# Kernel tuning notes

Measured on AMD Instinct MI355X. Metric: run time of the kernel, lower is better.

## Reference

```python
import jax, jax.numpy as jnp
import numpy as np

N_HEADS = 16
D_MODEL = 1024
D_K = D_MODEL // N_HEADS


def setup_inputs() -> dict:
    key = jax.random.key(0)
    ks = jax.random.split(key, 7)
    B, S = 2, 2048
    init = 0.02
    return {
        "query": jax.random.normal(ks[0], (B, S, D_MODEL), dtype=jnp.float32),
        "key": jax.random.normal(ks[1], (B, S, D_MODEL), dtype=jnp.float32),
        "value": jax.random.normal(ks[2], (B, S, D_MODEL), dtype=jnp.float32),
        "W_q": jax.random.normal(ks[3], (D_MODEL, D_MODEL), dtype=jnp.float32) * init,
        "W_k": jax.random.normal(ks[4], (D_MODEL, D_MODEL), dtype=jnp.float32) * init,
        "W_v": jax.random.normal(ks[5], (D_MODEL, D_MODEL), dtype=jnp.float32) * init,
        "W_o": jax.random.normal(ks[6], (D_MODEL, D_MODEL), dtype=jnp.float32) * init,
    }


def _split_heads(x):
    # (B, S, d_model) -> (B, H, S, d_k)
    B, S, _ = x.shape
    return x.reshape(B, S, N_HEADS, D_K).transpose(0, 2, 1, 3)


def reference(query, key, value, W_q, W_k, W_v, W_o):
    scale = jnp.sqrt(jnp.asarray(D_K, dtype=query.dtype))
    # torch Linear: y = x @ W.T
    Q = _split_heads(query @ W_q.T)   # (B,H,Sq,dk)
    K = _split_heads(key @ W_k.T)     # (B,H,Sk,dk)
    V = _split_heads(value @ W_v.T)   # (B,H,Sk,dk)
    scores = jnp.einsum("bhqd,bhkd->bhqk", Q, K) / scale
    attn = jax.nn.softmax(scores, axis=-1)           # (B,H,Sq,Sk); dropout p=0 -> identity
    attn_weights = attn.mean(axis=1)                 # (B,Sq,Sk) interpretable weights
    head_out = jnp.einsum("bhqk,bhkd->bqhd", attn, V)  # (B,Sq,H,dk)
    # NOTE: the original computes a head-gating (W_h) whose result is overwritten
    # by the concat below -> dead code, omitted.
    B, Sq = head_out.shape[0], head_out.shape[1]
    out = head_out.reshape(B, Sq, D_MODEL) @ W_o.T   # (B,Sq,d_model)
    return (out, attn_weights)
```

## Files before the change

### kernel.cpp

```cpp
#include <hip/hip_runtime.h>
#include <hip/hip_bf16.h>

#define Bq 2
#define Hh 16
#define Ss 2048
#define Dm 1024
#define Dk 64
#define QSC 0.18033688f

typedef _Float16 f16x8 __attribute__((ext_vector_type(8)));
typedef _Float16 f16x4 __attribute__((ext_vector_type(4)));
typedef _Float16 f16x2 __attribute__((ext_vector_type(2)));
typedef float    f32x4 __attribute__((ext_vector_type(4)));


__device__ __forceinline__ void gl_lds16(const void* g, void* lds) {
    __builtin_amdgcn_global_load_lds(
        (const __attribute__((address_space(1))) void*)g,
        (__attribute__((address_space(3))) void*)lds, 16, 0, 0);
}

extern "C" __device__ float __ocml_exp2_f32(float);

__device__ __forceinline__ float exp2_fast(float x) {
#if __has_builtin(__builtin_amdgcn_exp2f)
    return __builtin_amdgcn_exp2f(x);
#else
    return __ocml_exp2_f32(x);
#endif
}

__device__ __forceinline__ float rcp_fast(float x) {
#if __has_builtin(__builtin_amdgcn_rcpf)
    return __builtin_amdgcn_rcpf(x);
#else
    float r; asm("v_rcp_f32 %0, %1" : "=v"(r) : "v"(x)); return r;
#endif
}

__device__ __forceinline__ f16x2 pk_f16(float a, float b) {
    return __builtin_bit_cast(f16x2, __builtin_amdgcn_cvt_pkrtz(a, b));
}

__global__ __launch_bounds__(256) void convert_kernel(
    const float* __restrict__ q, const float* __restrict__ k,
    const float* __restrict__ v, const float* __restrict__ wq,
    const float* __restrict__ wk, const float* __restrict__ wv,
    const float* __restrict__ wo,
    _Float16* __restrict__ qd, _Float16* __restrict__ kd,
    _Float16* __restrict__ vd, _Float16* __restrict__ wd)
{
    int seg = blockIdx.y;
    const float* src; _Float16* dst; int n4;
    switch (seg) {
        case 0: src = q; dst = qd; n4 = 1048576; break;
        case 1: src = k; dst = kd; n4 = 1048576; break;
        case 2: src = v; dst = vd; n4 = 1048576; break;
        default:
            src = (seg == 3) ? wq : (seg == 4) ? wk : (seg == 5) ? wv : wo;
            dst = wd + (size_t)(seg - 3) * 1048576;
            n4 = 262144;
    }
    for (int i = blockIdx.x * 256 + threadIdx.x; i < n4; i += gridDim.x * 256) {
        float4 x = ((const float4*)src)[i];
        f16x4 h = {(_Float16)x.x, (_Float16)x.y, (_Float16)x.z, (_Float16)x.w};
        ((f16x4*)dst)[i] = h;
    }
}

__global__ __launch_bounds__(256) void gemm_qkv(
    const _Float16* __restrict__ qf, const _Float16* __restrict__ kf,
    const _Float16* __restrict__ vf, const _Float16* __restrict__ Wh,
    _Float16* __restrict__ Qd, _Float16* __restrict__ Kd,
    _Float16* __restrict__ Vd)
{
    __shared__ alignas(16) char smem[32768];
    _Float16* As = (_Float16*)smem;
    _Float16* Ws = (_Float16*)(smem + 8192);
    int z = blockIdx.z;
    const _Float16* A = (z == 0) ? qf : (z == 1) ? kf : vf;
    const _Float16* W = Wh + (size_t)z * (Dm * Dm);
    int t = threadIdx.x, lane = t & 63, w = t >> 6;
    int quad = lane >> 4, l15 = lane & 15;
    int wm = w & 1, wn = w >> 1;
    int orig = blockIdx.y * 8 + blockIdx.x;
    int wgid = (orig & 7) * 32 + (orig >> 3);
    int n0 = (wgid & 7) * 128, m0 = (wgid >> 3) * 128;

    f32x4 acc[4][4] = {};
    for (int k0 = 0; k0 < Dm; k0 += 32) {
        __syncthreads();
        for (int j = 0; j < 2; ++j) {
            int ca = w * 128 + j * 64 + lane;
            int row = ca >> 2, c8 = (ca & 3) * 8;
            gl_lds16(&A[(size_t)(m0 + row) * Dm + k0 + c8],
                     &As[(size_t)(w * 128 + j * 64) * 8]);
            gl_lds16(&W[(size_t)(n0 + row) * Dm + k0 + c8],
                     &Ws[(size_t)(w * 128 + j * 64) * 8]);
        }
        __syncthreads();
        f16x8 af[4], bf[4];
        for (int mi = 0; mi < 4; ++mi)
            af[mi] = *(const f16x8*)&As[(wm * 64 + mi * 16 + l15) * 32 + quad * 8];
        for (int ni = 0; ni < 4; ++ni)
            bf[ni] = *(const f16x8*)&Ws[(wn * 64 + ni * 16 + l15) * 32 + quad * 8];
        for (int mi = 0; mi < 4; ++mi)
            for (int ni = 0; ni < 4; ++ni)
                acc[mi][ni] = __builtin_amdgcn_mfma_f32_16x16x32_f16(
                    af[mi], bf[ni], acc[mi][ni], 0, 0, 0);
    }

    if (z == 2) {
        __syncthreads();
        for (int mi = 0; mi < 4; ++mi)
            for (int ni = 0; ni < 4; ++ni) {
                int n_l = wn * 64 + ni * 16 + l15;
                int m_b = wm * 64 + mi * 16 + quad * 4;
                f16x4 hv = {(_Float16)acc[mi][ni][0], (_Float16)acc[mi][ni][1],
                            (_Float16)acc[mi][ni][2], (_Float16)acc[mi][ni][3]};
                *(f16x4*)(smem + n_l * 256 + ((m_b * 2) ^ ((n_l & 7) << 4))) = hv;
            }
        __syncthreads();
        int b = m0 >> 11, sb = m0 & (Ss - 1);
        for (int p = 0; p < 8; ++p) {
            int cid = p * 256 + t;
            int rown = cid >> 4, c16 = cid & 15;
            f16x8 v = *(const f16x8*)(smem + rown * 256 +
                                      ((c16 * 16) ^ ((rown & 7) << 4)));
            int n = n0 + rown;
            int h = n >> 6, d = n & 63;
            *(f16x8*)&Vd[(((size_t)(b * Hh + h) * Dk + d) << 11) + sb + c16 * 8] = v;
        }
    } else {
        _Float16* Y = (z == 0) ? Qd : Kd;
        float osc = (z == 0) ? QSC : 1.0f;
        for (int mi = 0; mi < 4; ++mi)
            for (int ni = 0; ni < 4; ++ni)
                for (int r = 0; r < 4; ++r) {
                    int m = m0 + wm * 64 + mi * 16 + quad * 4 + r;
                    int n = n0 + wn * 64 + ni * 16 + l15;
                    int b = m >> 11, s = m & (Ss - 1);
                    int h = n >> 6,  d = n & 63;
                    Y[(((size_t)(b * Hh + h) * Ss + s) << 6) + d] =
                        (_Float16)(acc[mi][ni][r] * osc);
                }
    }
}

__global__ __launch_bounds__(256) void gemm_out(
    const _Float16* __restrict__ HO, const _Float16* __restrict__ Woh,
    float* __restrict__ out)
{
    __shared__ _Float16 As[128 * 32];
    __shared__ _Float16 Ws[64 * 32];
    int t = threadIdx.x, lane = t & 63, w = t >> 6;
    int quad = lane >> 4, l15 = lane & 15;
    int orig = blockIdx.y * 16 + blockIdx.x;
    int wgid = (orig & 7) * 64 + (orig >> 3);
    int n0 = (wgid & 15) * 64, m0 = (wgid >> 4) * 128;

    f32x4 acc[2][4] = {};
    for (int k0 = 0; k0 < Dm; k0 += 32) {
        __syncthreads();
        for (int j = 0; j < 2; ++j) {
            int ca = w * 128 + j * 64 + lane;
            int row = ca >> 2, c8 = (ca & 3) * 8;
            gl_lds16(&HO[(size_t)(m0 + row) * Dm + k0 + c8],
                     &As[(size_t)(w * 128 + j * 64) * 8]);
        }
        {
            int cw = w * 64 + lane;
            int row = cw >> 2, c8 = (cw & 3) * 8;
            gl_lds16(&Woh[(size_t)(n0 + row) * Dm + k0 + c8],
                     &Ws[(size_t)(w * 64) * 8]);
        }
        __syncthreads();
        f16x8 af[2], bf[4];
        for (int mi = 0; mi < 2; ++mi)
            af[mi] = *(const f16x8*)&As[(w * 32 + mi * 16 + l15) * 32 + quad * 8];
        for (int ni = 0; ni < 4; ++ni)
            bf[ni] = *(const f16x8*)&Ws[(ni * 16 + l15) * 32 + quad * 8];
        for (int mi = 0; mi < 2; ++mi)
            for (int ni = 0; ni < 4; ++ni)
                acc[mi][ni] = __builtin_amdgcn_mfma_f32_16x16x32_f16(
                    af[mi], bf[ni], acc[mi][ni], 0, 0, 0);
    }
    for (int mi = 0; mi < 2; ++mi)
        for (int ni = 0; ni < 4; ++ni)
            for (int r = 0; r < 4; ++r) {
                int m = m0 + w * 32 + mi * 16 + quad * 4 + r;
                int n = n0 + ni * 16 + l15;
                out[(size_t)m * Dm + n] = acc[mi][ni][r];
            }
}

__global__ __launch_bounds__(256) void flash_kernel(
    const _Float16* __restrict__ Qh, const _Float16* __restrict__ Kh,
    const _Float16* __restrict__ Vt, _Float16* __restrict__ Op,
    float* __restrict__ lp)
{
    __shared__ alignas(16) char Ks[8192];
    __shared__ alignas(16) char Vs[8192];
    __shared__ alignas(16) char Ps[4][4096];
    int t = threadIdx.x;
    int lane = t & 63, w = t >> 6;
    int quad = lane >> 4, l15 = lane & 15;
    int bh = blockIdx.x;
    int q0 = blockIdx.y * 128 + w * 32;
    int ks = blockIdx.z;
    int kt0 = ks * 16, kt1 = kt0 + 16;

    const _Float16* Qp = Qh + (size_t)bh * Ss * Dk;
    const _Float16* Kp = Kh + (size_t)bh * Ss * Dk;
    const _Float16* Vp = Vt + (size_t)bh * Dk * Ss;

    f16x8 qf[2][2];
#pragma unroll
    for (int qh = 0; qh < 2; ++qh)
#pragma unroll
        for (int kf = 0; kf < 2; ++kf)
            qf[qh][kf] = *(const f16x8*)
                &Qp[(size_t)(q0 + qh * 16 + l15) * Dk + kf * 32 + quad * 8];

    const _Float16 one = (_Float16)1.0f;
    const f16x8 ones = {one, one, one, one, one, one, one, one};

    int srow0 = t >> 3;
    int colh  = (t & 7) * 8;
    int sw0 = srow0 * 128 + ((colh * 2) ^ ((srow0 & 7) << 4));
    int sw1 = sw0 + 32 * 128;
    int swz = (l15 & 7) << 4;

    f16x8 kr0 = *(const f16x8*)&Kp[(size_t)(kt0 * 64 + srow0) * Dk + colh];
    f16x8 kr1 = *(const f16x8*)&Kp[(size_t)(kt0 * 64 + srow0 + 32) * Dk + colh];
    f16x8 vr0 = *(const f16x8*)&Vp[(size_t)srow0 * Ss + kt0 * 64 + colh];
    f16x8 vr1 = *(const f16x8*)&Vp[(size_t)(srow0 + 32) * Ss + kt0 * 64 + colh];

    f32x4 o_acc[2][4] = {};
    f32x4 l_acc[2] = {};
    char* Pw = Ps[w];

    for (int kt = kt0; kt < kt1; ++kt) {
        __syncthreads();
        *(f16x8*)(Ks + sw0) = kr0;
        *(f16x8*)(Ks + sw1) = kr1;
        *(f16x8*)(Vs + sw0) = vr0;
        *(f16x8*)(Vs + sw1) = vr1;
        if (kt + 1 < kt1) {
            kr0 = *(const f16x8*)&Kp[(size_t)((kt + 1) * 64 + srow0) * Dk + colh];
            kr1 = *(const f16x8*)&Kp[(size_t)((kt + 1) * 64 + srow0 + 32) * Dk + colh];
            vr0 = *(const f16x8*)&Vp[(size_t)srow0 * Ss + (kt + 1) * 64 + colh];
            vr1 = *(const f16x8*)&Vp[(size_t)(srow0 + 32) * Ss + (kt + 1) * 64 + colh];
        }
        __syncthreads();

#pragma unroll
        for (int nt = 0; nt < 4; ++nt) {
            const char* rb = Ks + ((nt * 16 + l15) << 7);
            f16x8 kf0 = *(const f16x8*)(rb + ((quad * 16) ^ swz));
            f16x8 kf1 = *(const f16x8*)(rb + ((64 + quad * 16) ^ swz));
#pragma unroll
            for (int qh = 0; qh < 2; ++qh) {
                f32x4 z = {};
                z = __builtin_amdgcn_mfma_f32_16x16x32_f16(kf0, qf[qh][0], z, 0, 0, 0);
                z = __builtin_amdgcn_mfma_f32_16x16x32_f16(kf1, qf[qh][1], z, 0, 0, 0);
                f16x2 h0 = pk_f16(exp2_fast(z[0]), exp2_fast(z[1]));
                f16x2 h1 = pk_f16(exp2_fast(z[2]), exp2_fast(z[3]));
                f16x4 hv = {h0[0], h0[1], h1[0], h1[1]};
                int prow = qh * 16 + l15;
                *(f16x4*)(Pw + prow * 128 +
                          (((nt * 32 + quad * 8)) ^ ((prow & 7) << 4))) = hv;
            }
        }

        f16x8 vf[4][2];
#pragma unroll
        for (int dt = 0; dt < 4; ++dt) {
            const char* rb = Vs + ((dt * 16 + l15) << 7);
            vf[dt][0] = *(const f16x8*)(rb + ((quad * 16) ^ swz));
            vf[dt][1] = *(const f16x8*)(rb + ((64 + quad * 16) ^ swz));
        }
#pragma unroll
        for (int qh = 0; qh < 2; ++qh) {
            const char* pr = Pw + ((qh * 16 + l15) << 7);
            f16x8 pf0 = *(const f16x8*)(pr + ((quad * 16) ^ swz));
            f16x8 pf1 = *(const f16x8*)(pr + ((64 + quad * 16) ^ swz));
            l_acc[qh] = __builtin_amdgcn_mfma_f32_16x16x32_f16(
                pf0, ones, l_acc[qh], 0, 0, 0);
            l_acc[qh] = __builtin_amdgcn_mfma_f32_16x16x32_f16(
                pf1, ones, l_acc[qh], 0, 0, 0);
#pragma unroll
            for (int dt = 0; dt < 4; ++dt) {
                o_acc[qh][dt] = __builtin_amdgcn_mfma_f32_16x16x32_f16(
                    pf0, vf[dt][0], o_acc[qh][dt], 0, 0, 0);
                o_acc[qh][dt] = __builtin_amdgcn_mfma_f32_16x16x32_f16(
                    pf1, vf[dt][1], o_acc[qh][dt], 0, 0, 0);
            }
        }
    }

    _Float16* Od = Op + (size_t)ks * (Bq * Hh * Ss * Dk) + (size_t)bh * Ss * Dk;
#pragma unroll
    for (int qh = 0; qh < 2; ++qh) {
#pragma unroll
        for (int dt = 0; dt < 4; ++dt)
#pragma unroll
            for (int r = 0; r < 4; ++r) {
                int q = q0 + qh * 16 + quad * 4 + r;
                Od[(size_t)q * Dk + dt * 16 + l15] = (_Float16)o_acc[qh][dt][r];
            }
        if (l15 == 0)
#pragma unroll
            for (int r = 0; r < 4; ++r)
                lp[(size_t)ks * 65536 + (size_t)bh * Ss + q0 + qh * 16 +
                   quad * 4 + r] = l_acc[qh][r];
    }
}

__global__ __launch_bounds__(256) void reduce_kernel(
    const _Float16* __restrict__ Op, const float* __restrict__ lp,
    _Float16* __restrict__ HO, float* __restrict__ lw)
{
    int i = blockIdx.x * 256 + threadIdx.x;
    int d4  = i & 15;
    int row = i >> 4;
    f16x4 a = ((const f16x4*)Op)[i];
    f16x4 b = ((const f16x4*)Op)[i + 1048576];
    float l = lp[row] + lp[65536 + row];
    float inv = rcp_fast(l);
    int bh = row >> 11, q = row & (Ss - 1);
    int b_ = bh >> 4,  h = bh & 15;
    f16x4 o;
    for (int j = 0; j < 4; ++j)
        o[j] = (_Float16)(((float)a[j] + (float)b[j]) * inv);
    *(f16x4*)&HO[((size_t)(b_ * Ss + q)) * Dm + h * Dk + d4 * 4] = o;
    if (d4 == 0) lw[row] = l;
}

__global__ __launch_bounds__(256) void attn_mean_kernel(
    const _Float16* __restrict__ Qh, const _Float16* __restrict__ Kh,
    const float* __restrict__ lw, float* __restrict__ out_attn)
{
    __shared__ alignas(16) char Ks[8192];
    int t = threadIdx.x;
    int lane = t & 63, w = t >> 6;
    int quad = lane >> 4, l15 = lane & 15;
    int k0 = blockIdx.x * 64;
    int q0 = blockIdx.y * 128;
    int b  = blockIdx.z;
    int qrow = q0 + w * 32;

    int srow0 = t >> 3;
    int colh  = (t & 7) * 8;
    int sw0 = srow0 * 128 + ((colh * 2) ^ ((srow0 & 7) << 4));
    int sw1 = sw0 + 32 * 128;
    int swz = (l15 & 7) << 4;

    f16x8 kr0, kr1, qn[2][2];
    float4 ln[2];
    {
        size_t base = (size_t)(b * Hh) * Ss;
        kr0 = *(const f16x8*)&Kh[(base + k0 + srow0) * Dk + colh];
        kr1 = *(const f16x8*)&Kh[(base + k0 + srow0 + 32) * Dk + colh];
#pragma unroll
        for (int qh = 0; qh < 2; ++qh) {
            qn[qh][0] = *(const f16x8*)&Qh[(base + qrow + qh * 16 + l15) * Dk + quad * 8];
            qn[qh][1] = *(const f16x8*)&Qh[(base + qrow + qh * 16 + l15) * Dk + 32 + quad * 8];
            ln[qh] = *(const float4*)&lw[base + qrow + qh * 16 + quad * 4];
        }
    }

    f32x4 acc[2][4] = {};
    for (int h = 0; h < Hh; ++h) {
        __syncthreads();
        *(f16x8*)(Ks + sw0) = kr0;
        *(f16x8*)(Ks + sw1) = kr1;
        f16x8 qf[2][2];
        float4 lv[2];
#pragma unroll
        for (int qh = 0; qh < 2; ++qh) {
            qf[qh][0] = qn[qh][0]; qf[qh][1] = qn[qh][1]; lv[qh] = ln[qh];
        }
        if (h < Hh - 1) {
            size_t base = (size_t)(b * Hh + h + 1) * Ss;
            kr0 = *(const f16x8*)&Kh[(base + k0 + srow0) * Dk + colh];
            kr1 = *(const f16x8*)&Kh[(base + k0 + srow0 + 32) * Dk + colh];
#pragma unroll
            for (int qh = 0; qh < 2; ++qh) {
                qn[qh][0] = *(const f16x8*)&Qh[(base + qrow + qh * 16 + l15) * Dk + quad * 8];
                qn[qh][1] = *(const f16x8*)&Qh[(base + qrow + qh * 16 + l15) * Dk + 32 + quad * 8];
                ln[qh] = *(const float4*)&lw[base + qrow + qh * 16 + quad * 4];
            }
        }
        __syncthreads();

        float ir[2][4];
#pragma unroll
        for (int qh = 0; qh < 2; ++qh) {
            ir[qh][0] = rcp_fast(lv[qh].x); ir[qh][1] = rcp_fast(lv[qh].y);
            ir[qh][2] = rcp_fast(lv[qh].z); ir[qh][3] = rcp_fast(lv[qh].w);
        }
#pragma unroll
        for (int nt = 0; nt < 4; ++nt) {
            const char* rb = Ks + ((nt * 16 + l15) << 7);
            f16x8 b0 = *(const f16x8*)(rb + ((quad * 16) ^ swz));
            f16x8 b1 = *(const f16x8*)(rb + ((64 + quad * 16) ^ swz));
#pragma unroll
            for (int qh = 0; qh < 2; ++qh) {
                f32x4 z = {};
                z = __builtin_amdgcn_mfma_f32_16x16x32_f16(qf[qh][0], b0, z, 0, 0, 0);
                z = __builtin_amdgcn_mfma_f32_16x16x32_f16(qf[qh][1], b1, z, 0, 0, 0);
#pragma unroll
                for (int r = 0; r < 4; ++r)
                    acc[qh][nt][r] += exp2_fast(z[r]) * ir[qh][r];
            }
        }
    }

#pragma unroll
    for (int qh = 0; qh < 2; ++qh)
#pragma unroll
        for (int nt = 0; nt < 4; ++nt)
#pragma unroll
            for (int r = 0; r < 4; ++r) {
                int q = qrow + qh * 16 + quad * 4 + r;
                out_attn[((size_t)(b * Ss + q)) * Ss + k0 + nt * 16 + l15] =
                    acc[qh][nt][r] * (1.0f / Hh);
            }
}

extern "C" void kernel_launch(void* const* d_in, const int* in_sizes, int n_in,
                              void* d_out, int out_size, void* d_ws, size_t ws_size,
                              hipStream_t stream) {
    const float* query = (const float*)d_in[0];
    const float* key   = (const float*)d_in[1];
    const float* value = (const float*)d_in[2];
    const float* Wq    = (const float*)d_in[3];
    const float* Wk    = (const float*)d_in[4];
    const float* Wv    = (const float*)d_in[5];
    const float* Wo    = (const float*)d_in[6];

    float* out      = (float*)d_out;
    float* attn_out = out + (size_t)4194304;

    _Float16* HO  = (_Float16*)attn_out;
    _Float16* qf  = (_Float16*)(attn_out + 2097152);
    _Float16* kf  = qf + 4194304;
    _Float16* vf  = kf + 4194304;
    _Float16* Op  = qf;
    float*    lp  = (float*)(Op + 2 * 4194304);

    _Float16* Qh = (_Float16*)d_ws;
    _Float16* Kh = Qh + (size_t)4194304;
    _Float16* Vt = Kh + (size_t)4194304;
    _Float16* Wh = Vt + (size_t)4194304;
    float*    lw = (float*)(Wh + (size_t)4194304);

    convert_kernel<<<dim3(256, 7), 256, 0, stream>>>(
        query, key, value, Wq, Wk, Wv, Wo, qf, kf, vf, Wh);

    gemm_qkv<<<dim3(8, 32, 3), 256, 0, stream>>>(qf, kf, vf, Wh, Qh, Kh, Vt);

    flash_kernel<<<dim3(Bq * Hh, Ss / 128, 2), 256, 0, stream>>>(Qh, Kh, Vt, Op, lp);

    reduce_kernel<<<4096, 256, 0, stream>>>(Op, lp, HO, lw);

    gemm_out<<<dim3(16, 32), 256, 0, stream>>>(HO, Wh + (size_t)3 * 1048576, out);

    attn_mean_kernel<<<dim3(Ss / 64, Ss / 128, Bq), 256, 0, stream>>>(
        Qh, Kh, lw, attn_out);
}
```

Baseline: 267.1 us.

## Merge output projection GEMM and attention-mean into one interleaved tail kernel

Merges the output-projection GEMM and the head-averaged attention-weights kernel into a single launch of 1536 blocks. Every third block does a GEMM tile and the rest do attention-mean tiles, so the two independent workloads run concurrently on the GPU. HO is moved from the attn_out region into the Vt workspace buffer, which reduce_kernel writes to after flash_kernel is done with V. This removes a serial kernel boundary and the tail effect between the two launches. The cost is a larger shared-memory footprint per block and mixed register pressure across both code paths.

```diff
diff --git a/kernel.cpp b/kernel.cpp
--- a/kernel.cpp
+++ b/kernel.cpp
@@ -147,53 +147,6 @@
     }
 }
 
-__global__ __launch_bounds__(256) void gemm_out(
-    const _Float16* __restrict__ HO, const _Float16* __restrict__ Woh,
-    float* __restrict__ out)
-{
-    __shared__ _Float16 As[128 * 32];
-    __shared__ _Float16 Ws[64 * 32];
-    int t = threadIdx.x, lane = t & 63, w = t >> 6;
-    int quad = lane >> 4, l15 = lane & 15;
-    int orig = blockIdx.y * 16 + blockIdx.x;
-    int wgid = (orig & 7) * 64 + (orig >> 3);
-    int n0 = (wgid & 15) * 64, m0 = (wgid >> 4) * 128;
-
-    f32x4 acc[2][4] = {};
-    for (int k0 = 0; k0 < Dm; k0 += 32) {
-        __syncthreads();
-        for (int j = 0; j < 2; ++j) {
-            int ca = w * 128 + j * 64 + lane;
-            int row = ca >> 2, c8 = (ca & 3) * 8;
-            gl_lds16(&HO[(size_t)(m0 + row) * Dm + k0 + c8],
-                     &As[(size_t)(w * 128 + j * 64) * 8]);
-        }
-        {
-            int cw = w * 64 + lane;
-            int row = cw >> 2, c8 = (cw & 3) * 8;
-            gl_lds16(&Woh[(size_t)(n0 + row) * Dm + k0 + c8],
-                     &Ws[(size_t)(w * 64) * 8]);
-        }
-        __syncthreads();
-        f16x8 af[2], bf[4];
-        for (int mi = 0; mi < 2; ++mi)
-            af[mi] = *(const f16x8*)&As[(w * 32 + mi * 16 + l15) * 32 + quad * 8];
-        for (int ni = 0; ni < 4; ++ni)
-            bf[ni] = *(const f16x8*)&Ws[(ni * 16 + l15) * 32 + quad * 8];
-        for (int mi = 0; mi < 2; ++mi)
-            for (int ni = 0; ni < 4; ++ni)
-                acc[mi][ni] = __builtin_amdgcn_mfma_f32_16x16x32_f16(
-                    af[mi], bf[ni], acc[mi][ni], 0, 0, 0);
-    }
-    for (int mi = 0; mi < 2; ++mi)
-        for (int ni = 0; ni < 4; ++ni)
-            for (int r = 0; r < 4; ++r) {
-                int m = m0 + w * 32 + mi * 16 + quad * 4 + r;
-                int n = n0 + ni * 16 + l15;
-                out[(size_t)m * Dm + n] = acc[mi][ni][r];
-            }
-}
-
 __global__ __launch_bounds__(256) void flash_kernel(
     const _Float16* __restrict__ Qh, const _Float16* __restrict__ Kh,
     const _Float16* __restrict__ Vt, _Float16* __restrict__ Op,
@@ -337,52 +290,74 @@
     if (d4 == 0) lw[row] = l;
 }
 
-__global__ __launch_bounds__(256) void attn_mean_kernel(
-    const _Float16* __restrict__ Qh, const _Float16* __restrict__ Kh,
-    const float* __restrict__ lw, float* __restrict__ out_attn)
+__global__ __launch_bounds__(256) void tail_kernel(
+    const _Float16* __restrict__ HO, const _Float16* __restrict__ Woh,
+    float* __restrict__ out, const _Float16* __restrict__ Qh,
+    const _Float16* __restrict__ Kh, const float* __restrict__ lw,
+    float* __restrict__ out_attn)
 {
-    __shared__ alignas(16) char Ks[8192];
-    int t = threadIdx.x;
-    int lane = t & 63, w = t >> 6;
+    __shared__ alignas(16) char smem[12288];
+    int id = blockIdx.x;
+    int t = threadIdx.x, lane = t & 63, w = t >> 6;
     int quad = lane >> 4, l15 = lane & 15;
-    int k0 = blockIdx.x * 64;
-    int q0 = blockIdx.y * 128;
-    int b  = blockIdx.z;
-    int qrow = q0 + w * 32;
-
-    int srow0 = t >> 3;
-    int colh  = (t & 7) * 8;
-    int sw0 = srow0 * 128 + ((colh * 2) ^ ((srow0 & 7) << 4));
-    int sw1 = sw0 + 32 * 128;
-    int swz = (l15 & 7) << 4;
-
-    f16x8 kr0, kr1, qn[2][2];
-    float4 ln[2];
-    {
-        size_t base = (size_t)(b * Hh) * Ss;
-        kr0 = *(const f16x8*)&Kh[(base + k0 + srow0) * Dk + colh];
-        kr1 = *(const f16x8*)&Kh[(base + k0 + srow0 + 32) * Dk + colh];
-#pragma unroll
-        for (int qh = 0; qh < 2; ++qh) {
-            qn[qh][0] = *(const f16x8*)&Qh[(base + qrow + qh * 16 + l15) * Dk + quad * 8];
-            qn[qh][1] = *(const f16x8*)&Qh[(base + qrow + qh * 16 + l15) * Dk + 32 + quad * 8];
-            ln[qh] = *(const float4*)&lw[base + qrow + qh * 16 + quad * 4];
-        }
-    }
-
-    f32x4 acc[2][4] = {};
-    for (int h = 0; h < Hh; ++h) {
-        __syncthreads();
-        *(f16x8*)(Ks + sw0) = kr0;
-        *(f16x8*)(Ks + sw1) = kr1;
-        f16x8 qf[2][2];
-        float4 lv[2];
-#pragma unroll
-        for (int qh = 0; qh < 2; ++qh) {
-            qf[qh][0] = qn[qh][0]; qf[qh][1] = qn[qh][1]; lv[qh] = ln[qh];
-        }
-        if (h < Hh - 1) {
-            size_t base = (size_t)(b * Hh + h + 1) * Ss;
+
+    if (id % 3 == 0) {
+        int go = id / 3;
+        _Float16* As = (_Float16*)smem;
+        _Float16* Ws = (_Float16*)(smem + 8192);
+        int n0 = (go & 15) * 64, m0 = (go >> 4) * 128;
+
+        f32x4 acc[2][4] = {};
+        for (int k0 = 0; k0 < Dm; k0 += 32) {
+            __syncthreads();
+            for (int j = 0; j < 2; ++j) {
+                int ca = w * 128 + j * 64 + lane;
+                int row = ca >> 2, c8 = (ca & 3) * 8;
+                gl_lds16(&HO[(size_t)(m0 + row) * Dm + k0 + c8],
+                         &As[(size_t)(w * 128 + j * 64) * 8]);
+            }
+            {
+                int cw = w * 64 + lane;
+                int row = cw >> 2, c8 = (cw & 3) * 8;
+                gl_lds16(&Woh[(size_t)(n0 + row) * Dm + k0 + c8],
+                         &Ws[(size_t)(w * 64) * 8]);
+            }
+            __syncthreads();
+            f16x8 af[2], bf[4];
+            for (int mi = 0; mi < 2; ++mi)
+                af[mi] = *(const f16x8*)&As[(w * 32 + mi * 16 + l15) * 32 + quad * 8];
+            for (int ni = 0; ni < 4; ++ni)
+                bf[ni] = *(const f16x8*)&Ws[(ni * 16 + l15) * 32 + quad * 8];
+            for (int mi = 0; mi < 2; ++mi)
+                for (int ni = 0; ni < 4; ++ni)
+                    acc[mi][ni] = __builtin_amdgcn_mfma_f32_16x16x32_f16(
+                        af[mi], bf[ni], acc[mi][ni], 0, 0, 0);
+        }
+        for (int mi = 0; mi < 2; ++mi)
+            for (int ni = 0; ni < 4; ++ni)
+                for (int r = 0; r < 4; ++r) {
+                    int m = m0 + w * 32 + mi * 16 + quad * 4 + r;
+                    int n = n0 + ni * 16 + l15;
+                    out[(size_t)m * Dm + n] = acc[mi][ni][r];
+                }
+    } else {
+        int am = id - id / 3 - 1;
+        char* Ks = smem;
+        int k0 = (am & 31) * 64;
+        int q0 = ((am >> 5) & 15) * 128;
+        int b  = am >> 9;
+        int qrow = q0 + w * 32;
+
+        int srow0 = t >> 3;
+        int colh  = (t & 7) * 8;
+        int sw0 = srow0 * 128 + ((colh * 2) ^ ((srow0 & 7) << 4));
+        int sw1 = sw0 + 32 * 128;
+        int swz = (l15 & 7) << 4;
+
+        f16x8 kr0, kr1, qn[2][2];
+        float4 ln[2];
+        {
+            size_t base = (size_t)(b * Hh) * Ss;
             kr0 = *(const f16x8*)&Kh[(base + k0 + srow0) * Dk + colh];
             kr1 = *(const f16x8*)&Kh[(base + k0 + srow0 + 32) * Dk + colh];
 #pragma unroll
@@ -392,41 +367,65 @@
                 ln[qh] = *(const float4*)&lw[base + qrow + qh * 16 + quad * 4];
             }
         }
-        __syncthreads();
-
-        float ir[2][4];
-#pragma unroll
-        for (int qh = 0; qh < 2; ++qh) {
-            ir[qh][0] = rcp_fast(lv[qh].x); ir[qh][1] = rcp_fast(lv[qh].y);
-            ir[qh][2] = rcp_fast(lv[qh].z); ir[qh][3] = rcp_fast(lv[qh].w);
-        }
-#pragma unroll
-        for (int nt = 0; nt < 4; ++nt) {
-            const char* rb = Ks + ((nt * 16 + l15) << 7);
-            f16x8 b0 = *(const f16x8*)(rb + ((quad * 16) ^ swz));
-            f16x8 b1 = *(const f16x8*)(rb + ((64 + quad * 16) ^ swz));
+
+        f32x4 acc[2][4] = {};
+        for (int h = 0; h < Hh; ++h) {
+            __syncthreads();
+            *(f16x8*)(Ks + sw0) = kr0;
+            *(f16x8*)(Ks + sw1) = kr1;
+            f16x8 qf[2][2];
+            float4 lv[2];
 #pragma unroll
             for (int qh = 0; qh < 2; ++qh) {
-                f32x4 z = {};
-                z = __builtin_amdgcn_mfma_f32_16x16x32_f16(qf[qh][0], b0, z, 0, 0, 0);
-                z = __builtin_amdgcn_mfma_f32_16x16x32_f16(qf[qh][1], b1, z, 0, 0, 0);
-#pragma unroll
-                for (int r = 0; r < 4; ++r)
-                    acc[qh][nt][r] += exp2_fast(z[r]) * ir[qh][r];
-            }
-        }
-    }
-
-#pragma unroll
-    for (int qh = 0; qh < 2; ++qh)
-#pragma unroll
-        for (int nt = 0; nt < 4; ++nt)
-#pragma unroll
-            for (int r = 0; r < 4; ++r) {
-                int q = qrow + qh * 16 + quad * 4 + r;
-                out_attn[((size_t)(b * Ss + q)) * Ss + k0 + nt * 16 + l15] =
-                    acc[qh][nt][r] * (1.0f / Hh);
-            }
+                qf[qh][0] = qn[qh][0]; qf[qh][1] = qn[qh][1]; lv[qh] = ln[qh];
+            }
+            if (h < Hh - 1) {
+                size_t base = (size_t)(b * Hh + h + 1) * Ss;
+                kr0 = *(const f16x8*)&Kh[(base + k0 + srow0) * Dk + colh];
+                kr1 = *(const f16x8*)&Kh[(base + k0 + srow0 + 32) * Dk + colh];
+#pragma unroll
+                for (int qh = 0; qh < 2; ++qh) {
+                    qn[qh][0] = *(const f16x8*)&Qh[(base + qrow + qh * 16 + l15) * Dk + quad * 8];
+                    qn[qh][1] = *(const f16x8*)&Qh[(base + qrow + qh * 16 + l15) * Dk + 32 + quad * 8];
+                    ln[qh] = *(const float4*)&lw[base + qrow + qh * 16 + quad * 4];
+                }
+            }
+            __syncthreads();
+
+            float ir[2][4];
+#pragma unroll
+            for (int qh = 0; qh < 2; ++qh) {
+                ir[qh][0] = rcp_fast(lv[qh].x); ir[qh][1] = rcp_fast(lv[qh].y);
+                ir[qh][2] = rcp_fast(lv[qh].z); ir[qh][3] = rcp_fast(lv[qh].w);
+            }
+#pragma unroll
+            for (int nt = 0; nt < 4; ++nt) {
+                const char* rb = Ks + ((nt * 16 + l15) << 7);
+                f16x8 b0 = *(const f16x8*)(rb + ((quad * 16) ^ swz));
+                f16x8 b1 = *(const f16x8*)(rb + ((64 + quad * 16) ^ swz));
+#pragma unroll
+                for (int qh = 0; qh < 2; ++qh) {
+                    f32x4 z = {};
+                    z = __builtin_amdgcn_mfma_f32_16x16x32_f16(qf[qh][0], b0, z, 0, 0, 0);
+                    z = __builtin_amdgcn_mfma_f32_16x16x32_f16(qf[qh][1], b1, z, 0, 0, 0);
+#pragma unroll
+                    for (int r = 0; r < 4; ++r)
+                        acc[qh][nt][r] += exp2_fast(z[r]) * ir[qh][r];
+                }
+            }
+        }
+
+#pragma unroll
+        for (int qh = 0; qh < 2; ++qh)
+#pragma unroll
+            for (int nt = 0; nt < 4; ++nt)
+#pragma unroll
+                for (int r = 0; r < 4; ++r) {
+                    int q = qrow + qh * 16 + quad * 4 + r;
+                    out_attn[((size_t)(b * Ss + q)) * Ss + k0 + nt * 16 + l15] =
+                        acc[qh][nt][r] * (1.0f / Hh);
+                }
+    }
 }
 
 extern "C" void kernel_launch(void* const* d_in, const int* in_sizes, int n_in,
@@ -443,7 +442,6 @@
     float* out      = (float*)d_out;
     float* attn_out = out + (size_t)4194304;
 
-    _Float16* HO  = (_Float16*)attn_out;
     _Float16* qf  = (_Float16*)(attn_out + 2097152);
     _Float16* kf  = qf + 4194304;
     _Float16* vf  = kf + 4194304;
@@ -455,6 +453,7 @@
     _Float16* Vt = Kh + (size_t)4194304;
     _Float16* Wh = Vt + (size_t)4194304;
     float*    lw = (float*)(Wh + (size_t)4194304);
+    _Float16* HO = Vt;
 
     convert_kernel<<<dim3(256, 7), 256, 0, stream>>>(
         query, key, value, Wq, Wk, Wv, Wo, qf, kf, vf, Wh);
@@ -465,8 +464,6 @@
 
     reduce_kernel<<<4096, 256, 0, stream>>>(Op, lp, HO, lw);
 
-    gemm_out<<<dim3(16, 32), 256, 0, stream>>>(HO, Wh + (size_t)3 * 1048576, out);
-
-    attn_mean_kernel<<<dim3(Ss / 64, Ss / 128, Bq), 256, 0, stream>>>(
-        Qh, Kh, lw, attn_out);
-}
+    tail_kernel<<<1536, 256, 0, stream>>>(
+        HO, Wh + (size_t)3 * 1048576, out, Qh, Kh, lw, attn_out);
+}
```

Measured after the change: 256.9 us. 1.04x faster.
